# Kernel tuning notes

Measured on AMD Instinct MI355X. Metric: run time of the kernel, lower is better.

Reference implementation:

```python
import jax, jax.numpy as jnp
import numpy as np

NEG_INF = -1e30


def setup_inputs() -> dict:
    key = jax.random.key(0)
    ks = jax.random.split(key, 11)
    b, n, d = 4, 2048, 1024
    scale = 1.0 / np.sqrt(d)
    inp = {
        "q": jax.random.normal(ks[0], (b, n, d), jnp.float32),
        "k": jax.random.normal(ks[1], (b, n, d), jnp.float32),
        "v": jax.random.normal(ks[2], (b, n, d), jnp.float32),
        # nn.Linear params: weight [out, in], bias [out]
        "Wq": jax.random.normal(ks[3], (d, d), jnp.float32) * scale,
        "bq": jnp.zeros((d,), jnp.float32),
        "Wk": jax.random.normal(ks[4], (d, d), jnp.float32) * scale,
        "bk": jnp.zeros((d,), jnp.float32),
        "Wv": jax.random.normal(ks[5], (d, d), jnp.float32) * scale,
        "bv": jnp.zeros((d,), jnp.float32),
        "Wo": jax.random.normal(ks[6], (d, d), jnp.float32) * scale,
        "bo": jnp.zeros((d,), jnp.float32),
    }
    return inp


def reference(q, k, v, Wq, bq, Wk, bk, Wv, bv, Wo, bo):
    # Faithful to source: the multi-head reshape/transpose results are never
    # assigned, so attention runs single-headed over full n_embd vectors.
    b, n, d = q.shape
    qp = q @ Wq.T + bq  # [b, n, d]
    kp = k @ Wk.T + bk
    vp = v @ Wv.T + bv
    scale = jnp.asarray(1.0 / d, qp.dtype) ** 0.5  # sqrt(1/d)
    att = jnp.einsum('bnd,bmd->bnm', qp, kp) * scale  # [b, n, n]
    causal = jnp.tril(jnp.ones((n, n), bool))          # block_size tril sliced to n
    att = jnp.where(causal[None, :, :], att, NEG_INF)
    att = jax.nn.softmax(att, axis=-1)  # dropout p=0.0 -> identity
    y = att @ vp                        # [b, n, d]
    # source bug reproduced: transpose(1,2) then reshape(b, n, d)
    y = jnp.swapaxes(y, 1, 2).reshape(b, n, d)
    y = y @ Wo.T + bo
    return y
```

## Files before the change

kernel.cpp:

```cpp
#include <hip/hip_runtime.h>
#include <hip/hip_bf16.h>
#include <stdint.h>

typedef __bf16 bf16_t;
typedef __bf16 bf16x8 __attribute__((ext_vector_type(8)));
typedef __bf16 bf16x4 __attribute__((ext_vector_type(4)));
typedef float f32x4 __attribute__((ext_vector_type(4)));

#define GLD_LDS16(src, dst)                                                              \
  __builtin_amdgcn_global_load_lds((const __attribute__((address_space(1))) void*)(src), \
                                   (__attribute__((address_space(3))) void*)(dst), 16, 0, 0)

struct CvtArgs {
  const float* src[7];
  bf16_t* dst[7];
  long n4[7];
};

__global__ __launch_bounds__(256) void cvt_all(CvtArgs a) {
  const int seg = blockIdx.y;
  const float* __restrict__ in = a.src[seg];
  bf16_t* __restrict__ out = a.dst[seg];
  const long n4 = a.n4[seg];
  long i = (long)blockIdx.x * blockDim.x + threadIdx.x;
  const long stride = (long)gridDim.x * blockDim.x;
  for (; i < n4; i += stride) {
    float4 v = ((const float4*)in)[i];
    bf16x4 o;
    o[0] = (bf16_t)v.x; o[1] = (bf16_t)v.y; o[2] = (bf16_t)v.z; o[3] = (bf16_t)v.w;
    ((bf16x4*)out)[i] = o;
  }
}

__global__ __launch_bounds__(256) void transpose_bf16(const bf16_t* __restrict__ in,
                                                      bf16_t* __restrict__ out,
                                                      int rows, int cols, long sIn, long sOut) {
  __shared__ bf16_t tile[32][33];
  const int z = blockIdx.z;
  in  += (long)z * sIn;
  out += (long)z * sOut;
  const int c0 = blockIdx.x << 5, r0 = blockIdx.y << 5;
  const int tc = threadIdx.x & 31, tr = threadIdx.x >> 5;
#pragma unroll
  for (int it = 0; it < 4; ++it)
    tile[tr + it * 8][tc] = in[(long)(r0 + tr + it * 8) * cols + c0 + tc];
  __syncthreads();
#pragma unroll
  for (int it = 0; it < 4; ++it)
    out[(long)(c0 + tr + it * 8) * rows + r0 + tc] = tile[tc][tr + it * 8];
}

__global__ __launch_bounds__(256) void softmax_causal(bf16_t* __restrict__ S, int n, long sB) {
  const int i = blockIdx.x;
  const int z = blockIdx.y;
  bf16_t* row = S + (long)z * sB + (long)i * n;
  const int t = threadIdx.x;
  const int j0 = t << 3;

  bf16x8 vv = ((const bf16x8*)row)[t];
  float vals[8];
  float mx = -3.0e38f;
#pragma unroll
  for (int e = 0; e < 8; ++e) {
    float v = (j0 + e <= i) ? (float)vv[e] : -3.0e38f;
    vals[e] = v;
    mx = fmaxf(mx, v);
  }
#pragma unroll
  for (int off = 32; off; off >>= 1) mx = fmaxf(mx, __shfl_xor(mx, off));
  __shared__ float redm[4];
  if ((t & 63) == 0) redm[t >> 6] = mx;
  __syncthreads();
  mx = fmaxf(fmaxf(redm[0], redm[1]), fmaxf(redm[2], redm[3]));

  float sum = 0.f;
#pragma unroll
  for (int e = 0; e < 8; ++e) {
    float p = (j0 + e <= i) ? __expf(vals[e] - mx) : 0.f;
    vals[e] = p;
    sum += p;
  }
#pragma unroll
  for (int off = 32; off; off >>= 1) sum += __shfl_xor(sum, off);
  __shared__ float reds[4];
  if ((t & 63) == 0) reds[t >> 6] = sum;
  __syncthreads();
  sum = reds[0] + reds[1] + reds[2] + reds[3];
  const float inv = 1.0f / sum;

  bf16x8 o;
#pragma unroll
  for (int e = 0; e < 8; ++e) o[e] = (bf16_t)(vals[e] * inv);
  ((bf16x8*)row)[t] = o;
}

template <bool BF16_OUT, bool BIAS, bool KBOUND>
__device__ __forceinline__ void gemm_body(const bf16_t* __restrict__ A,
                                          const bf16_t* __restrict__ B,
                                          const float* __restrict__ bias,
                                          void* __restrict__ Cout,
                                          int N, int K, float alpha,
                                          int m0, int n0) {
  int KT = K >> 5;
  if (KBOUND) {
    int kb = (n0 + 128) >> 5;
    if (kb < KT) KT = kb;
  }

  __shared__ __align__(16) bf16_t As[128 * 32];
  __shared__ __align__(16) bf16_t Bs[128 * 32];

  const int t = threadIdx.x;
  const int l = t & 63;
  const int w = t >> 6;
  const int wr = w >> 1, wc = w & 1;

  const int c0 = t, c1 = t + 256;
  const bf16_t* a_src0 = A + (long)(m0 + (c0 >> 2)) * K + ((c0 & 3) << 3);
  const bf16_t* a_src1 = A + (long)(m0 + (c1 >> 2)) * K + ((c1 & 3) << 3);
  const bf16_t* b_src0 = B + (long)(n0 + (c0 >> 2)) * K + ((c0 & 3) << 3);
  const bf16_t* b_src1 = B + (long)(n0 + (c1 >> 2)) * K + ((c1 & 3) << 3);
  char* const asb = (char*)As;
  char* const bsb = (char*)Bs;
  char* const a_dst0 = asb + w * 1024;
  char* const a_dst1 = asb + 4096 + w * 1024;
  char* const b_dst0 = bsb + w * 1024;
  char* const b_dst1 = bsb + 4096 + w * 1024;

  const int r16 = l & 15, kg = l >> 4;
  int aoff[4], boff[4];
#pragma unroll
  for (int mi = 0; mi < 4; ++mi) aoff[mi] = (((wr * 64 + mi * 16 + r16) * 32) + kg * 8) * 2;
#pragma unroll
  for (int ni = 0; ni < 4; ++ni) boff[ni] = (((wc * 64 + ni * 16 + r16) * 32) + kg * 8) * 2;

  f32x4 acc[4][4] = {};

  for (int kt = 0; kt < KT; ++kt) {
    __syncthreads();
    GLD_LDS16(a_src0, a_dst0);
    GLD_LDS16(a_src1, a_dst1);
    GLD_LDS16(b_src0, b_dst0);
    GLD_LDS16(b_src1, b_dst1);
    a_src0 += 32; a_src1 += 32; b_src0 += 32; b_src1 += 32;
    __syncthreads();

    bf16x8 af[4], bfr[4];
#pragma unroll
    for (int mi = 0; mi < 4; ++mi) af[mi] = *(const bf16x8*)(asb + aoff[mi]);
#pragma unroll
    for (int ni = 0; ni < 4; ++ni) bfr[ni] = *(const bf16x8*)(bsb + boff[ni]);
#pragma unroll
    for (int mi = 0; mi < 4; ++mi)
#pragma unroll
      for (int ni = 0; ni < 4; ++ni)
        acc[mi][ni] = __builtin_amdgcn_mfma_f32_16x16x32_bf16(af[mi], bfr[ni], acc[mi][ni], 0, 0, 0);
  }

  const int rowbase = m0 + wr * 64 + ((l >> 4) << 2);
  const int colbase = n0 + wc * 64 + (l & 15);
  if constexpr (BF16_OUT) {
    bf16_t* C = (bf16_t*)Cout;
#pragma unroll
    for (int mi = 0; mi < 4; ++mi)
#pragma unroll
      for (int ni = 0; ni < 4; ++ni) {
        const int col = colbase + ni * 16;
        float badd = 0.f;
        if constexpr (BIAS) badd = bias[col];
#pragma unroll
        for (int j = 0; j < 4; ++j) {
          float v = acc[mi][ni][j] * alpha + badd;
          C[(long)(rowbase + mi * 16 + j) * N + col] = (bf16_t)v;
        }
      }
  } else {
    float* C = (float*)Cout;
#pragma unroll
    for (int mi = 0; mi < 4; ++mi)
#pragma unroll
      for (int ni = 0; ni < 4; ++ni) {
        const int col = colbase + ni * 16;
        float badd = 0.f;
        if constexpr (BIAS) badd = bias[col];
#pragma unroll
        for (int j = 0; j < 4; ++j) {
          float v = acc[mi][ni][j] * alpha + badd;
          C[(long)(rowbase + mi * 16 + j) * N + col] = v;
        }
      }
  }
}

__device__ __forceinline__ void xcd_remap(int& bx, int& by, int& bz) {
  const int gx = gridDim.x, gy = gridDim.y;
  int lin = (blockIdx.z * gy + blockIdx.y) * gx + blockIdx.x;
  const int nwg = gx * gy * (int)gridDim.z;
  lin = (lin & 7) * (nwg >> 3) + (lin >> 3);
  bx = lin % gx;
  const int rem = lin / gx;
  by = rem % gy;
  bz = rem / gy;
}

template <bool BF16_OUT, bool BIAS, bool CAUSAL_SKIP, bool KBOUND>
__global__ __launch_bounds__(256, 4) void gemm_bt(const bf16_t* __restrict__ A,
                                                  const bf16_t* __restrict__ B,
                                                  const float* __restrict__ bias,
                                                  void* __restrict__ Cout,
                                                  int N, int K, float alpha,
                                                  long sAb, long sBb, long sCb, int eltC) {
  int bx, by, bz;
  xcd_remap(bx, by, bz);
  const int m0 = by << 7, n0 = bx << 7;
  if (CAUSAL_SKIP && n0 > m0 + 127) return;
  gemm_body<BF16_OUT, BIAS, KBOUND>(A + (long)bz * sAb, B + (long)bz * sBb, bias,
                                    (char*)Cout + (long)bz * sCb * eltC, N, K, alpha, m0, n0);
}

struct QkvArgs {
  const bf16_t* A[3];
  const bf16_t* B[3];
  const float* bias[3];
  bf16_t* C[3];
};

__global__ __launch_bounds__(256, 4) void gemm_qkv(QkvArgs a, int N, int K) {
  int bx, by, bz;
  xcd_remap(bx, by, bz);
  gemm_body<true, true, false>(a.A[bz], a.B[bz], a.bias[bz], a.C[bz], N, K, 1.0f,
                               by << 7, bx << 7);
}

extern "C" void kernel_launch(void* const* d_in, const int* in_sizes, int n_in,
                              void* d_out, int out_size, void* d_ws, size_t ws_size,
                              hipStream_t stream) {
  const int b = 4, n = 2048, d = 1024;
  const long nd  = (long)n * d;
  const long bn  = (long)b * n;
  const long bnd = bn * d;
  const long ddl = (long)d * d;
  const long nn  = (long)n * n;

  const float* q  = (const float*)d_in[0];
  const float* k  = (const float*)d_in[1];
  const float* v  = (const float*)d_in[2];
  const float* Wq = (const float*)d_in[3];
  const float* bq = (const float*)d_in[4];
  const float* Wk = (const float*)d_in[5];
  const float* bk = (const float*)d_in[6];
  const float* Wv = (const float*)d_in[7];
  const float* bv = (const float*)d_in[8];
  const float* Wo = (const float*)d_in[9];
  const float* bo = (const float*)d_in[10];

  bf16_t* ws  = (bf16_t*)d_ws;
  bf16_t* qB  = ws;
  bf16_t* kB  = qB + bnd;
  bf16_t* vB  = kB + bnd;
  bf16_t* WqB = vB + bnd;
  bf16_t* WkB = WqB + ddl;
  bf16_t* WvB = WkB + ddl;
  bf16_t* WoB = WvB + ddl;
  bf16_t* qpB = WoB + ddl;
  bf16_t* kpB = qpB + bnd;
  bf16_t* vpB = kpB + bnd;
  bf16_t* vpT = vpB + bnd;
  bf16_t* S   = vpT + bnd;
  bf16_t* yT  = S + (long)b * nn;
  const size_t need = (size_t)(8 * bnd + 4 * ddl + (long)b * nn) * 2;
  if (ws_size < need) return;

  dim3 blk(256);

  CvtArgs ca;
  ca.src[0] = q;  ca.dst[0] = qB;  ca.n4[0] = bnd / 4;
  ca.src[1] = k;  ca.dst[1] = kB;  ca.n4[1] = bnd / 4;
  ca.src[2] = v;  ca.dst[2] = vB;  ca.n4[2] = bnd / 4;
  ca.src[3] = Wq; ca.dst[3] = WqB; ca.n4[3] = ddl / 4;
  ca.src[4] = Wk; ca.dst[4] = WkB; ca.n4[4] = ddl / 4;
  ca.src[5] = Wv; ca.dst[5] = WvB; ca.n4[5] = ddl / 4;
  ca.src[6] = Wo; ca.dst[6] = WoB; ca.n4[6] = ddl / 4;
  cvt_all<<<dim3(512, 7), blk, 0, stream>>>(ca);

  QkvArgs qa;
  qa.A[0] = qB; qa.B[0] = WqB; qa.bias[0] = bq; qa.C[0] = qpB;
  qa.A[1] = kB; qa.B[1] = WkB; qa.bias[1] = bk; qa.C[1] = kpB;
  qa.A[2] = vB; qa.B[2] = WvB; qa.bias[2] = bv; qa.C[2] = vpB;
  gemm_qkv<<<dim3(d / 128, bn / 128, 3), blk, 0, stream>>>(qa, d, d);

  transpose_bf16<<<dim3(d / 32, n / 32, b), blk, 0, stream>>>(vpB, vpT, n, d, nd, nd);

  gemm_bt<true, false, true, false><<<dim3(n / 128, n / 128, b), blk, 0, stream>>>(
      qpB, kpB, nullptr, S, n, d, 0.03125f, nd, nd, nn, 2);

  softmax_causal<<<dim3(n, b), blk, 0, stream>>>(S, n, nn);

  gemm_bt<true, false, false, true><<<dim3(n / 128, d / 128, b), blk, 0, stream>>>(
      vpT, S, nullptr, yT, n, n, 1.f, nd, nn, nd, 2);

  gemm_bt<false, true, false, false><<<dim3(d / 128, bn / 128, 1), blk, 0, stream>>>(
      yT, WoB, bo, (float*)d_out, d, d, 1.f, 0, 0, 0, 4);
}
```

Baseline: 221.9 us.

## Add 256x256 pipelined 8-wave GEMM for QKV and QK^T, fuse V transpose

Introduces a new 512-thread GEMM kernel using 256x256 output tiles, a 128KB double-buffered LDS staging scheme with swizzled offsets, explicit vmcnt waits and barriers, and setprio around MFMA bursts. It is used for the QKV projection and the causal QK^T scores. The V projection epilogue now writes the transposed layout directly, which removes the separate transpose kernel and its buffer. Larger tiles raise operand reuse and cut global traffic, but they lower occupancy and make causal skipping coarser.

```diff
diff --git a/kernel.cpp b/kernel.cpp
--- a/kernel.cpp
+++ b/kernel.cpp
@@ -10,6 +10,13 @@
 #define GLD_LDS16(src, dst)                                                              \
   __builtin_amdgcn_global_load_lds((const __attribute__((address_space(1))) void*)(src), \
                                    (__attribute__((address_space(3))) void*)(dst), 16, 0, 0)
+
+#define BAR() __builtin_amdgcn_s_barrier()
+#define LGKM0() asm volatile("s_waitcnt lgkmcnt(0)" ::: "memory")
+#define VMC6() asm volatile("s_waitcnt vmcnt(6)" ::: "memory")
+#define VMC0() asm volatile("s_waitcnt vmcnt(0)" ::: "memory")
+
+__device__ __forceinline__ int swz(int x) { return x ^ (((x >> 9) & 1) << 5); }
 
 struct CvtArgs {
   const float* src[7];
@@ -32,24 +39,6 @@
   }
 }
 
-__global__ __launch_bounds__(256) void transpose_bf16(const bf16_t* __restrict__ in,
-                                                      bf16_t* __restrict__ out,
-                                                      int rows, int cols, long sIn, long sOut) {
-  __shared__ bf16_t tile[32][33];
-  const int z = blockIdx.z;
-  in  += (long)z * sIn;
-  out += (long)z * sOut;
-  const int c0 = blockIdx.x << 5, r0 = blockIdx.y << 5;
-  const int tc = threadIdx.x & 31, tr = threadIdx.x >> 5;
-#pragma unroll
-  for (int it = 0; it < 4; ++it)
-    tile[tr + it * 8][tc] = in[(long)(r0 + tr + it * 8) * cols + c0 + tc];
-  __syncthreads();
-#pragma unroll
-  for (int it = 0; it < 4; ++it)
-    out[(long)(c0 + tr + it * 8) * rows + r0 + tc] = tile[tc][tr + it * 8];
-}
-
 __global__ __launch_bounds__(256) void softmax_causal(bf16_t* __restrict__ S, int n, long sB) {
   const int i = blockIdx.x;
   const int z = blockIdx.y;
@@ -92,6 +81,235 @@
 #pragma unroll
   for (int e = 0; e < 8; ++e) o[e] = (bf16_t)(vals[e] * inv);
   ((bf16x8*)row)[t] = o;
+}
+
+__device__ __forceinline__ void xcd_remap(int& bx, int& by, int& bz) {
+  const int gx = gridDim.x, gy = gridDim.y;
+  int lin = (blockIdx.z * gy + blockIdx.y) * gx + blockIdx.x;
+  const int nwg = gx * gy * (int)gridDim.z;
+  lin = (lin & 7) * (nwg >> 3) + (lin >> 3);
+  bx = lin % gx;
+  const int rem = lin / gx;
+  by = rem % gy;
+  bz = rem / gy;
+}
+
+struct G8Args {
+  const bf16_t* A[3];
+  const bf16_t* W[3];
+  const float* bias[3];
+  bf16_t* C[3];
+  long sA, sB, sC;
+};
+
+template <int HALF, int BUF>
+__device__ __forceinline__ void stage8(char* lds, const bf16_t* srcH, const int (&soff)[2],
+                                       int wid, int tile) {
+  const bf16_t* s = srcH + tile * 64;
+  char* d = lds + (HALF >= 2 ? 65536 : 0) + BUF * 32768 + (HALF & 1) * 16384 + wid * 2048;
+  GLD_LDS16(s + soff[0], d);
+  GLD_LDS16(s + soff[1], d + 1024);
+}
+
+template <int BUF, int QM>
+__device__ __forceinline__ void rdA(char* lds, const int (&aoffp)[4][2], bf16x8 (&af)[4][2]) {
+  char* b = lds + BUF * 32768 + QM * 16384;
+#pragma unroll
+  for (int mi = 0; mi < 4; ++mi)
+#pragma unroll
+    for (int kk = 0; kk < 2; ++kk) af[mi][kk] = *(const bf16x8*)(b + aoffp[mi][kk]);
+}
+
+template <int BUF, int QN>
+__device__ __forceinline__ void rdB(char* lds, const int (&boffp)[2][2], bf16x8 (&bf)[2][2]) {
+  char* b = lds + 65536 + BUF * 32768 + QN * 16384;
+#pragma unroll
+  for (int ni = 0; ni < 2; ++ni)
+#pragma unroll
+    for (int kk = 0; kk < 2; ++kk) bf[ni][kk] = *(const bf16x8*)(b + boffp[ni][kk]);
+}
+
+template <int QM, int QN>
+__device__ __forceinline__ void mm16(f32x4 (&acc)[2][2][4][2], const bf16x8 (&af)[4][2],
+                                     const bf16x8 (&bf)[2][2]) {
+  __builtin_amdgcn_s_setprio(1);
+#pragma unroll
+  for (int mi = 0; mi < 4; ++mi)
+#pragma unroll
+    for (int ni = 0; ni < 2; ++ni)
+#pragma unroll
+      for (int kk = 0; kk < 2; ++kk)
+        acc[QM][QN][mi][ni] = __builtin_amdgcn_mfma_f32_16x16x32_bf16(
+            af[mi][kk], bf[ni][kk], acc[QM][QN][mi][ni], 0, 0, 0);
+  __builtin_amdgcn_s_setprio(0);
+}
+
+template <int MODE>
+__global__ __launch_bounds__(512, 2) void gemm8(G8Args ga) {
+  int bx, by, bz;
+  xcd_remap(bx, by, bz);
+  const int m0 = by << 8, n0 = bx << 8;
+  if (MODE == 1 && n0 > m0 + 255) return;
+
+  const int K = 1024, NT = 16;
+  const bf16_t* A;
+  const bf16_t* B;
+  const float* bias = nullptr;
+  if (MODE == 0) {
+    A = ga.A[bz]; B = ga.W[bz]; bias = ga.bias[bz];
+  } else {
+    A = ga.A[0] + (long)bz * ga.sA;
+    B = ga.W[0] + (long)bz * ga.sB;
+  }
+
+  __shared__ __align__(16) char lds[131072];
+
+  const int t = threadIdx.x;
+  const int wid = t >> 6, l = t & 63;
+  const int wm = wid >> 2, wn = wid & 3;
+  const int ri16 = l & 15, kg = l >> 4;
+
+  int soff[2];
+#pragma unroll
+  for (int i = 0; i < 2; ++i) {
+    const int sub = wid * 2 + i;
+    const int ri = l >> 2;
+    const int cq = (l & 3) ^ ((ri & 8) >> 2);
+    const int r = (sub >> 1) * 16 + ri;
+    const int c = (sub & 1) * 32 + cq * 8;
+    soff[i] = r * K + c;
+  }
+  const bf16_t* srcA0 = A + (long)m0 * K;
+  const bf16_t* srcA1 = A + (long)(m0 + 128) * K;
+  const bf16_t* srcB0 = B + (long)n0 * K;
+  const bf16_t* srcB1 = B + (long)(n0 + 128) * K;
+
+  int aoffp[4][2], boffp[2][2];
+#pragma unroll
+  for (int mi = 0; mi < 4; ++mi)
+#pragma unroll
+    for (int kk = 0; kk < 2; ++kk)
+      aoffp[mi][kk] = swz((wm * 4 + mi) * 2048 + kk * 1024 + ri16 * 64 + kg * 16);
+#pragma unroll
+  for (int ni = 0; ni < 2; ++ni)
+#pragma unroll
+    for (int kk = 0; kk < 2; ++kk)
+      boffp[ni][kk] = swz((wn * 2 + ni) * 2048 + kk * 1024 + ri16 * 64 + kg * 16);
+
+  f32x4 acc[2][2][4][2] = {};
+  bf16x8 af[4][2], bf0[2][2], bf1[2][2];
+
+  stage8<0, 0>(lds, srcA0, soff, wid, 0);
+  stage8<2, 0>(lds, srcB0, soff, wid, 0);
+  stage8<3, 0>(lds, srcB1, soff, wid, 0);
+  stage8<1, 0>(lds, srcA1, soff, wid, 0);
+  stage8<0, 1>(lds, srcA0, soff, wid, 1);
+  stage8<2, 1>(lds, srcB0, soff, wid, 1);
+  stage8<3, 1>(lds, srcB1, soff, wid, 1);
+  VMC6();
+  BAR();
+
+  for (int tt = 0; tt < NT; tt += 2) {
+    const bool hasNext = (tt + 2) < NT;
+    rdA<0, 0>(lds, aoffp, af);
+    rdB<0, 0>(lds, boffp, bf0);
+    stage8<1, 1>(lds, srcA1, soff, wid, tt + 1);
+    BAR(); LGKM0();
+    mm16<0, 0>(acc, af, bf0);
+    BAR();
+    rdB<0, 1>(lds, boffp, bf1);
+    if (hasNext) stage8<0, 0>(lds, srcA0, soff, wid, tt + 2);
+    BAR(); LGKM0();
+    mm16<0, 1>(acc, af, bf1);
+    BAR();
+    rdA<0, 1>(lds, aoffp, af);
+    if (hasNext) stage8<2, 0>(lds, srcB0, soff, wid, tt + 2);
+    BAR(); LGKM0();
+    mm16<1, 0>(acc, af, bf0);
+    BAR();
+    if (hasNext) stage8<3, 0>(lds, srcB1, soff, wid, tt + 2);
+    BAR(); LGKM0();
+    mm16<1, 1>(acc, af, bf1);
+    if (hasNext) { VMC6(); } else { VMC0(); }
+    BAR();
+    rdA<1, 0>(lds, aoffp, af);
+    rdB<1, 0>(lds, boffp, bf0);
+    if (hasNext) stage8<1, 0>(lds, srcA1, soff, wid, tt + 2);
+    BAR(); LGKM0();
+    mm16<0, 0>(acc, af, bf0);
+    BAR();
+    rdB<1, 1>(lds, boffp, bf1);
+    if (hasNext) stage8<0, 1>(lds, srcA0, soff, wid, tt + 3);
+    BAR(); LGKM0();
+    mm16<0, 1>(acc, af, bf1);
+    BAR();
+    rdA<1, 1>(lds, aoffp, af);
+    if (hasNext) stage8<2, 1>(lds, srcB0, soff, wid, tt + 3);
+    BAR(); LGKM0();
+    mm16<1, 0>(acc, af, bf0);
+    BAR();
+    if (hasNext) stage8<3, 1>(lds, srcB1, soff, wid, tt + 3);
+    BAR(); LGKM0();
+    mm16<1, 1>(acc, af, bf1);
+    if (hasNext) { VMC6(); }
+    BAR();
+  }
+
+  if (MODE == 0) {
+    if (bz < 2) {
+      bf16_t* C = ga.C[bz];
+#pragma unroll
+      for (int qm = 0; qm < 2; ++qm)
+#pragma unroll
+        for (int qn = 0; qn < 2; ++qn)
+#pragma unroll
+          for (int mi = 0; mi < 4; ++mi)
+#pragma unroll
+            for (int ni = 0; ni < 2; ++ni) {
+              const int col = n0 + qn * 128 + wn * 32 + ni * 16 + ri16;
+              const int row0 = m0 + qm * 128 + wm * 64 + mi * 16 + kg * 4;
+              const float badd = bias[col];
+#pragma unroll
+              for (int j = 0; j < 4; ++j)
+                C[(long)(row0 + j) * 1024 + col] = (bf16_t)(acc[qm][qn][mi][ni][j] + badd);
+            }
+    } else {
+      bf16_t* C = ga.C[2];
+#pragma unroll
+      for (int qm = 0; qm < 2; ++qm)
+#pragma unroll
+        for (int qn = 0; qn < 2; ++qn)
+#pragma unroll
+          for (int mi = 0; mi < 4; ++mi)
+#pragma unroll
+            for (int ni = 0; ni < 2; ++ni) {
+              const int col = n0 + qn * 128 + wn * 32 + ni * 16 + ri16;
+              const int row0 = m0 + qm * 128 + wm * 64 + mi * 16 + kg * 4;
+              const float badd = bias[col];
+              const int batch = row0 >> 11, nr = row0 & 2047;
+              bf16x4 o;
+#pragma unroll
+              for (int j = 0; j < 4; ++j) o[j] = (bf16_t)(acc[qm][qn][mi][ni][j] + badd);
+              *(bf16x4*)(C + (long)batch * (2048 * 1024) + (long)col * 2048 + nr) = o;
+            }
+    }
+  } else {
+    bf16_t* C = ga.C[0] + (long)bz * ga.sC;
+#pragma unroll
+    for (int qm = 0; qm < 2; ++qm)
+#pragma unroll
+      for (int qn = 0; qn < 2; ++qn)
+#pragma unroll
+        for (int mi = 0; mi < 4; ++mi)
+#pragma unroll
+          for (int ni = 0; ni < 2; ++ni) {
+            const int col = n0 + qn * 128 + wn * 32 + ni * 16 + ri16;
+            const int row0 = m0 + qm * 128 + wm * 64 + mi * 16 + kg * 4;
+#pragma unroll
+            for (int j = 0; j < 4; ++j)
+              C[(long)(row0 + j) * 2048 + col] = (bf16_t)(acc[qm][qn][mi][ni][j] * 0.03125f);
+          }
+  }
 }
 
 template <bool BF16_OUT, bool BIAS, bool KBOUND>
@@ -192,18 +410,7 @@
   }
 }
 
-__device__ __forceinline__ void xcd_remap(int& bx, int& by, int& bz) {
-  const int gx = gridDim.x, gy = gridDim.y;
-  int lin = (blockIdx.z * gy + blockIdx.y) * gx + blockIdx.x;
-  const int nwg = gx * gy * (int)gridDim.z;
-  lin = (lin & 7) * (nwg >> 3) + (lin >> 3);
-  bx = lin % gx;
-  const int rem = lin / gx;
-  by = rem % gy;
-  bz = rem / gy;
-}
-
-template <bool BF16_OUT, bool BIAS, bool CAUSAL_SKIP, bool KBOUND>
+template <bool BF16_OUT, bool BIAS, bool KBOUND>
 __global__ __launch_bounds__(256, 4) void gemm_bt(const bf16_t* __restrict__ A,
                                                   const bf16_t* __restrict__ B,
                                                   const float* __restrict__ bias,
@@ -213,23 +420,8 @@
   int bx, by, bz;
   xcd_remap(bx, by, bz);
   const int m0 = by << 7, n0 = bx << 7;
-  if (CAUSAL_SKIP && n0 > m0 + 127) return;
   gemm_body<BF16_OUT, BIAS, KBOUND>(A + (long)bz * sAb, B + (long)bz * sBb, bias,
                                     (char*)Cout + (long)bz * sCb * eltC, N, K, alpha, m0, n0);
-}
-
-struct QkvArgs {
-  const bf16_t* A[3];
-  const bf16_t* B[3];
-  const float* bias[3];
-  bf16_t* C[3];
-};
-
-__global__ __launch_bounds__(256, 4) void gemm_qkv(QkvArgs a, int N, int K) {
-  int bx, by, bz;
-  xcd_remap(bx, by, bz);
-  gemm_body<true, true, false>(a.A[bz], a.B[bz], a.bias[bz], a.C[bz], N, K, 1.0f,
-                               by << 7, bx << 7);
 }
 
 extern "C" void kernel_launch(void* const* d_in, const int* in_sizes, int n_in,
@@ -264,11 +456,10 @@
   bf16_t* WoB = WvB + ddl;
   bf16_t* qpB = WoB + ddl;
   bf16_t* kpB = qpB + bnd;
-  bf16_t* vpB = kpB + bnd;
-  bf16_t* vpT = vpB + bnd;
+  bf16_t* vpT = kpB + bnd;
   bf16_t* S   = vpT + bnd;
   bf16_t* yT  = S + (long)b * nn;
-  const size_t need = (size_t)(8 * bnd + 4 * ddl + (long)b * nn) * 2;
+  const size_t need = (size_t)(7 * bnd + 4 * ddl + (long)b * nn) * 2;
   if (ws_size < need) return;
 
   dim3 blk(256);
@@ -283,22 +474,22 @@
   ca.src[6] = Wo; ca.dst[6] = WoB; ca.n4[6] = ddl / 4;
   cvt_all<<<dim3(512, 7), blk, 0, stream>>>(ca);
 
-  QkvArgs qa;
-  qa.A[0] = qB; qa.B[0] = WqB; qa.bias[0] = bq; qa.C[0] = qpB;
-  qa.A[1] = kB; qa.B[1] = WkB; qa.bias[1] = bk; qa.C[1] = kpB;
-  qa.A[2] = vB; qa.B[2] = WvB; qa.bias[2] = bv; qa.C[2] = vpB;
-  gemm_qkv<<<dim3(d / 128, bn / 128, 3), blk, 0, stream>>>(qa, d, d);
-
-  transpose_bf16<<<dim3(d / 32, n / 32, b), blk, 0, stream>>>(vpB, vpT, n, d, nd, nd);
-
-  gemm_bt<true, false, true, false><<<dim3(n / 128, n / 128, b), blk, 0, stream>>>(
-      qpB, kpB, nullptr, S, n, d, 0.03125f, nd, nd, nn, 2);
+  G8Args qa = {};
+  qa.A[0] = qB; qa.W[0] = WqB; qa.bias[0] = bq; qa.C[0] = qpB;
+  qa.A[1] = kB; qa.W[1] = WkB; qa.bias[1] = bk; qa.C[1] = kpB;
+  qa.A[2] = vB; qa.W[2] = WvB; qa.bias[2] = bv; qa.C[2] = vpT;
+  gemm8<0><<<dim3(d / 256, bn / 256, 3), dim3(512), 0, stream>>>(qa);
+
+  G8Args sa = {};
+  sa.A[0] = qpB; sa.W[0] = kpB; sa.C[0] = S;
+  sa.sA = nd; sa.sB = nd; sa.sC = nn;
+  gemm8<1><<<dim3(n / 256, n / 256, b), dim3(512), 0, stream>>>(sa);
 
   softmax_causal<<<dim3(n, b), blk, 0, stream>>>(S, n, nn);
 
-  gemm_bt<true, false, false, true><<<dim3(n / 128, d / 128, b), blk, 0, stream>>>(
+  gemm_bt<true, false, true><<<dim3(n / 128, d / 128, b), blk, 0, stream>>>(
       vpT, S, nullptr, yT, n, n, 1.f, nd, nn, nd, 2);
 
-  gemm_bt<false, true, false, false><<<dim3(d / 128, bn / 128, 1), blk, 0, stream>>>(
+  gemm_bt<false, true, false><<<dim3(d / 128, bn / 128, 1), blk, 0, stream>>>(
       yT, WoB, bo, (float*)d_out, d, d, 1.f, 0, 0, 0, 4);
 }
```

Measured after the change: 220.9 us. About the same (-0.4%).

## Fuse fp32-to-bf16 activation conversion and V transpose into QKV GEMM

Applied to the files above, without the earlier changes.

The QKV projection GEMM now loads fp32 activations straight into LDS with direct global-to-LDS loads and converts them to bf16 on the fly. This removes the separate conversion pass over q, k and v and its intermediate bf16 buffers. The V projection writes its output already transposed, so the standalone transpose kernel is dropped. Softmax also skips loading and storing columns beyond the causal 128-block boundary. In exchange, the GEMM moves twice the A-operand bytes through LDS and does extra conversion work inside the inner loop.

```diff
diff --git a/kernel.cpp b/kernel.cpp
--- a/kernel.cpp
+++ b/kernel.cpp
@@ -12,9 +12,9 @@
                                    (__attribute__((address_space(3))) void*)(dst), 16, 0, 0)
 
 struct CvtArgs {
-  const float* src[7];
-  bf16_t* dst[7];
-  long n4[7];
+  const float* src[4];
+  bf16_t* dst[4];
+  long n4[4];
 };
 
 __global__ __launch_bounds__(256) void cvt_all(CvtArgs a) {
@@ -32,39 +32,25 @@
   }
 }
 
-__global__ __launch_bounds__(256) void transpose_bf16(const bf16_t* __restrict__ in,
-                                                      bf16_t* __restrict__ out,
-                                                      int rows, int cols, long sIn, long sOut) {
-  __shared__ bf16_t tile[32][33];
-  const int z = blockIdx.z;
-  in  += (long)z * sIn;
-  out += (long)z * sOut;
-  const int c0 = blockIdx.x << 5, r0 = blockIdx.y << 5;
-  const int tc = threadIdx.x & 31, tr = threadIdx.x >> 5;
-#pragma unroll
-  for (int it = 0; it < 4; ++it)
-    tile[tr + it * 8][tc] = in[(long)(r0 + tr + it * 8) * cols + c0 + tc];
-  __syncthreads();
-#pragma unroll
-  for (int it = 0; it < 4; ++it)
-    out[(long)(c0 + tr + it * 8) * rows + r0 + tc] = tile[tc][tr + it * 8];
-}
-
 __global__ __launch_bounds__(256) void softmax_causal(bf16_t* __restrict__ S, int n, long sB) {
   const int i = blockIdx.x;
   const int z = blockIdx.y;
   bf16_t* row = S + (long)z * sB + (long)i * n;
   const int t = threadIdx.x;
   const int j0 = t << 3;
-
-  bf16x8 vv = ((const bf16x8*)row)[t];
+  const int jmax = ((i >> 7) + 1) << 7;
+  const bool active = j0 < jmax;
+
   float vals[8];
   float mx = -3.0e38f;
-#pragma unroll
-  for (int e = 0; e < 8; ++e) {
-    float v = (j0 + e <= i) ? (float)vv[e] : -3.0e38f;
-    vals[e] = v;
-    mx = fmaxf(mx, v);
+  if (active) {
+    bf16x8 vv = ((const bf16x8*)row)[t];
+#pragma unroll
+    for (int e = 0; e < 8; ++e) {
+      float v = (j0 + e <= i) ? (float)vv[e] : -3.0e38f;
+      vals[e] = v;
+      mx = fmaxf(mx, v);
+    }
   }
 #pragma unroll
   for (int off = 32; off; off >>= 1) mx = fmaxf(mx, __shfl_xor(mx, off));
@@ -74,11 +60,13 @@
   mx = fmaxf(fmaxf(redm[0], redm[1]), fmaxf(redm[2], redm[3]));
 
   float sum = 0.f;
-#pragma unroll
-  for (int e = 0; e < 8; ++e) {
-    float p = (j0 + e <= i) ? __expf(vals[e] - mx) : 0.f;
-    vals[e] = p;
-    sum += p;
+  if (active) {
+#pragma unroll
+    for (int e = 0; e < 8; ++e) {
+      float p = (j0 + e <= i) ? __expf(vals[e] - mx) : 0.f;
+      vals[e] = p;
+      sum += p;
+    }
   }
 #pragma unroll
   for (int off = 32; off; off >>= 1) sum += __shfl_xor(sum, off);
@@ -88,19 +76,41 @@
   sum = reds[0] + reds[1] + reds[2] + reds[3];
   const float inv = 1.0f / sum;
 
-  bf16x8 o;
-#pragma unroll
-  for (int e = 0; e < 8; ++e) o[e] = (bf16_t)(vals[e] * inv);
-  ((bf16x8*)row)[t] = o;
-}
-
-template <bool BF16_OUT, bool BIAS, bool KBOUND>
-__device__ __forceinline__ void gemm_body(const bf16_t* __restrict__ A,
-                                          const bf16_t* __restrict__ B,
-                                          const float* __restrict__ bias,
-                                          void* __restrict__ Cout,
-                                          int N, int K, float alpha,
-                                          int m0, int n0) {
+  if (active) {
+    bf16x8 o;
+#pragma unroll
+    for (int e = 0; e < 8; ++e) o[e] = (bf16_t)(vals[e] * inv);
+    ((bf16x8*)row)[t] = o;
+  }
+}
+
+__device__ __forceinline__ void xcd_remap(int& bx, int& by, int& bz) {
+  const int gx = gridDim.x, gy = gridDim.y;
+  int lin = (blockIdx.z * gy + blockIdx.y) * gx + blockIdx.x;
+  const int nwg = gx * gy * (int)gridDim.z;
+  lin = (lin & 7) * (nwg >> 3) + (lin >> 3);
+  bx = lin % gx;
+  const int rem = lin / gx;
+  by = rem % gy;
+  bz = rem / gy;
+}
+
+template <bool BF16_OUT, bool BIAS, bool CAUSAL_SKIP, bool KBOUND>
+__global__ __launch_bounds__(256, 4) void gemm_bt(const bf16_t* __restrict__ Ag,
+                                                  const bf16_t* __restrict__ Bg,
+                                                  const float* __restrict__ bias,
+                                                  void* __restrict__ Cout,
+                                                  int N, int K, float alpha,
+                                                  long sAb, long sBb, long sCb, int eltC) {
+  int bx, by, bz;
+  xcd_remap(bx, by, bz);
+  const int m0 = by << 7, n0 = bx << 7;
+  if (CAUSAL_SKIP && n0 > m0 + 127) return;
+
+  const bf16_t* A = Ag + (long)bz * sAb;
+  const bf16_t* B = Bg + (long)bz * sBb;
+  void* Cv = (char*)Cout + (long)bz * sCb * eltC;
+
   int KT = K >> 5;
   if (KBOUND) {
     int kb = (n0 + 128) >> 5;
@@ -160,7 +170,7 @@
   const int rowbase = m0 + wr * 64 + ((l >> 4) << 2);
   const int colbase = n0 + wc * 64 + (l & 15);
   if constexpr (BF16_OUT) {
-    bf16_t* C = (bf16_t*)Cout;
+    bf16_t* C = (bf16_t*)Cv;
 #pragma unroll
     for (int mi = 0; mi < 4; ++mi)
 #pragma unroll
@@ -175,7 +185,7 @@
         }
       }
   } else {
-    float* C = (float*)Cout;
+    float* C = (float*)Cv;
 #pragma unroll
     for (int mi = 0; mi < 4; ++mi)
 #pragma unroll
@@ -192,44 +202,119 @@
   }
 }
 
-__device__ __forceinline__ void xcd_remap(int& bx, int& by, int& bz) {
-  const int gx = gridDim.x, gy = gridDim.y;
-  int lin = (blockIdx.z * gy + blockIdx.y) * gx + blockIdx.x;
-  const int nwg = gx * gy * (int)gridDim.z;
-  lin = (lin & 7) * (nwg >> 3) + (lin >> 3);
-  bx = lin % gx;
-  const int rem = lin / gx;
-  by = rem % gy;
-  bz = rem / gy;
-}
-
-template <bool BF16_OUT, bool BIAS, bool CAUSAL_SKIP, bool KBOUND>
-__global__ __launch_bounds__(256, 4) void gemm_bt(const bf16_t* __restrict__ A,
-                                                  const bf16_t* __restrict__ B,
-                                                  const float* __restrict__ bias,
-                                                  void* __restrict__ Cout,
-                                                  int N, int K, float alpha,
-                                                  long sAb, long sBb, long sCb, int eltC) {
+struct QkvArgsF {
+  const float* A[3];
+  const bf16_t* W[3];
+  const float* bias[3];
+  bf16_t* C[3];
+};
+
+__global__ __launch_bounds__(256, 4) void gemm_qkv_f32dma(QkvArgsF ga, int N, int K) {
   int bx, by, bz;
   xcd_remap(bx, by, bz);
   const int m0 = by << 7, n0 = bx << 7;
-  if (CAUSAL_SKIP && n0 > m0 + 127) return;
-  gemm_body<BF16_OUT, BIAS, KBOUND>(A + (long)bz * sAb, B + (long)bz * sBb, bias,
-                                    (char*)Cout + (long)bz * sCb * eltC, N, K, alpha, m0, n0);
-}
-
-struct QkvArgs {
-  const bf16_t* A[3];
-  const bf16_t* B[3];
-  const float* bias[3];
-  bf16_t* C[3];
-};
-
-__global__ __launch_bounds__(256, 4) void gemm_qkv(QkvArgs a, int N, int K) {
-  int bx, by, bz;
-  xcd_remap(bx, by, bz);
-  gemm_body<true, true, false>(a.A[bz], a.B[bz], a.bias[bz], a.C[bz], N, K, 1.0f,
-                               by << 7, bx << 7);
+
+  const float* __restrict__ A = ga.A[bz];
+  const bf16_t* __restrict__ B = ga.W[bz];
+  const float* __restrict__ bias = ga.bias[bz];
+  const int KT = K >> 5;
+
+  __shared__ __align__(16) char lds[24576];
+  char* const asb = lds;
+  char* const bsb = lds + 16384;
+
+  const int t = threadIdx.x;
+  const int l = t & 63;
+  const int w = t >> 6;
+  const int wr = w >> 1, wc = w & 1;
+
+  const float* a_src[4];
+#pragma unroll
+  for (int i = 0; i < 4; ++i) {
+    const int c = i * 256 + t;
+    const int row = c >> 3;
+    const int lo16 = (c & 7) ^ (row & 7);
+    a_src[i] = A + (long)(m0 + row) * K + lo16 * 4;
+  }
+  const int c0 = t, c1 = t + 256;
+  const bf16_t* b_src0 = B + (long)(n0 + (c0 >> 2)) * K + ((c0 & 3) << 3);
+  const bf16_t* b_src1 = B + (long)(n0 + (c1 >> 2)) * K + ((c1 & 3) << 3);
+  char* const b_dst0 = bsb + w * 1024;
+  char* const b_dst1 = bsb + 4096 + w * 1024;
+
+  const int r16 = l & 15, kg = l >> 4;
+  int aoff[4], boff[4];
+#pragma unroll
+  for (int mi = 0; mi < 4; ++mi) {
+    const int row = wr * 64 + mi * 16 + r16;
+    aoff[mi] = (row * 128 + kg * 32) ^ ((row & 7) << 4);
+  }
+#pragma unroll
+  for (int ni = 0; ni < 4; ++ni) boff[ni] = (((wc * 64 + ni * 16 + r16) * 32) + kg * 8) * 2;
+
+  f32x4 acc[4][4] = {};
+
+  for (int kt = 0; kt < KT; ++kt) {
+    __syncthreads();
+#pragma unroll
+    for (int i = 0; i < 4; ++i) {
+      GLD_LDS16(a_src[i], asb + i * 4096 + w * 1024);
+      a_src[i] += 32;
+    }
+    GLD_LDS16(b_src0, b_dst0);
+    GLD_LDS16(b_src1, b_dst1);
+    b_src0 += 32; b_src1 += 32;
+    __syncthreads();
+
+    bf16x8 af[4], bfr[4];
+#pragma unroll
+    for (int mi = 0; mi < 4; ++mi) {
+      f32x4 lo4 = *(const f32x4*)(asb + aoff[mi]);
+      f32x4 hi4 = *(const f32x4*)(asb + (aoff[mi] ^ 16));
+      af[mi][0] = (bf16_t)lo4[0]; af[mi][1] = (bf16_t)lo4[1];
+      af[mi][2] = (bf16_t)lo4[2]; af[mi][3] = (bf16_t)lo4[3];
+      af[mi][4] = (bf16_t)hi4[0]; af[mi][5] = (bf16_t)hi4[1];
+      af[mi][6] = (bf16_t)hi4[2]; af[mi][7] = (bf16_t)hi4[3];
+    }
+#pragma unroll
+    for (int ni = 0; ni < 4; ++ni) bfr[ni] = *(const bf16x8*)(bsb + boff[ni]);
+#pragma unroll
+    for (int mi = 0; mi < 4; ++mi)
+#pragma unroll
+      for (int ni = 0; ni < 4; ++ni)
+        acc[mi][ni] = __builtin_amdgcn_mfma_f32_16x16x32_bf16(af[mi], bfr[ni], acc[mi][ni], 0, 0, 0);
+  }
+
+  const int rowbase = m0 + wr * 64 + ((l >> 4) << 2);
+  const int colbase = n0 + wc * 64 + (l & 15);
+  if (bz < 2) {
+    bf16_t* C = ga.C[bz];
+#pragma unroll
+    for (int mi = 0; mi < 4; ++mi)
+#pragma unroll
+      for (int ni = 0; ni < 4; ++ni) {
+        const int col = colbase + ni * 16;
+        const float badd = bias[col];
+#pragma unroll
+        for (int j = 0; j < 4; ++j)
+          C[(long)(rowbase + mi * 16 + j) * N + col] = (bf16_t)(acc[mi][ni][j] + badd);
+      }
+  } else {
+    bf16_t* C = ga.C[2];
+#pragma unroll
+    for (int mi = 0; mi < 4; ++mi)
+#pragma unroll
+      for (int ni = 0; ni < 4; ++ni) {
+        const int col = colbase + ni * 16;
+        const float badd = bias[col];
+        const int row0 = rowbase + mi * 16;
+        const int batch = row0 >> 11, nr = row0 & 2047;
+        bf16x4 o;
+#pragma unroll
+        for (int j = 0; j < 4; ++j) o[j] = (bf16_t)(acc[mi][ni][j] + badd);
+        *(bf16x4*)(C + (long)batch * (2048 * 1024) + (long)col * 2048 + nr) = o;
+      }
+  }
 }
 
 extern "C" void kernel_launch(void* const* d_in, const int* in_sizes, int n_in,
@@ -255,41 +340,32 @@
   const float* bo = (const float*)d_in[10];
 
   bf16_t* ws  = (bf16_t*)d_ws;
-  bf16_t* qB  = ws;
-  bf16_t* kB  = qB + bnd;
-  bf16_t* vB  = kB + bnd;
-  bf16_t* WqB = vB + bnd;
+  bf16_t* WqB = ws;
   bf16_t* WkB = WqB + ddl;
   bf16_t* WvB = WkB + ddl;
   bf16_t* WoB = WvB + ddl;
   bf16_t* qpB = WoB + ddl;
   bf16_t* kpB = qpB + bnd;
-  bf16_t* vpB = kpB + bnd;
-  bf16_t* vpT = vpB + bnd;
+  bf16_t* vpT = kpB + bnd;
   bf16_t* S   = vpT + bnd;
   bf16_t* yT  = S + (long)b * nn;
-  const size_t need = (size_t)(8 * bnd + 4 * ddl + (long)b * nn) * 2;
+  const size_t need = (size_t)(4 * ddl + 4 * bnd + (long)b * nn) * 2;
   if (ws_size < need) return;
 
   dim3 blk(256);
 
   CvtArgs ca;
-  ca.src[0] = q;  ca.dst[0] = qB;  ca.n4[0] = bnd / 4;
-  ca.src[1] = k;  ca.dst[1] = kB;  ca.n4[1] = bnd / 4;
-  ca.src[2] = v;  ca.dst[2] = vB;  ca.n4[2] = bnd / 4;
-  ca.src[3] = Wq; ca.dst[3] = WqB; ca.n4[3] = ddl / 4;
-  ca.src[4] = Wk; ca.dst[4] = WkB; ca.n4[4] = ddl / 4;
-  ca.src[5] = Wv; ca.dst[5] = WvB; ca.n4[5] = ddl / 4;
-  ca.src[6] = Wo; ca.dst[6] = WoB; ca.n4[6] = ddl / 4;
-  cvt_all<<<dim3(512, 7), blk, 0, stream>>>(ca);
-
-  QkvArgs qa;
-  qa.A[0] = qB; qa.B[0] = WqB; qa.bias[0] = bq; qa.C[0] = qpB;
-  qa.A[1] = kB; qa.B[1] = WkB; qa.bias[1] = bk; qa.C[1] = kpB;
-  qa.A[2] = vB; qa.B[2] = WvB; qa.bias[2] = bv; qa.C[2] = vpB;
-  gemm_qkv<<<dim3(d / 128, bn / 128, 3), blk, 0, stream>>>(qa, d, d);
-
-  transpose_bf16<<<dim3(d / 32, n / 32, b), blk, 0, stream>>>(vpB, vpT, n, d, nd, nd);
+  ca.src[0] = Wq; ca.dst[0] = WqB; ca.n4[0] = ddl / 4;
+  ca.src[1] = Wk; ca.dst[1] = WkB; ca.n4[1] = ddl / 4;
+  ca.src[2] = Wv; ca.dst[2] = WvB; ca.n4[2] = ddl / 4;
+  ca.src[3] = Wo; ca.dst[3] = WoB; ca.n4[3] = ddl / 4;
+  cvt_all<<<dim3(256, 4), blk, 0, stream>>>(ca);
+
+  QkvArgsF qa;
+  qa.A[0] = q; qa.W[0] = WqB; qa.bias[0] = bq; qa.C[0] = qpB;
+  qa.A[1] = k; qa.W[1] = WkB; qa.bias[1] = bk; qa.C[1] = kpB;
+  qa.A[2] = v; qa.W[2] = WvB; qa.bias[2] = bv; qa.C[2] = vpT;
+  gemm_qkv_f32dma<<<dim3(d / 128, bn / 128, 3), blk, 0, stream>>>(qa, d, d);
 
   gemm_bt<true, false, true, false><<<dim3(n / 128, n / 128, b), blk, 0, stream>>>(
       qpB, kpB, nullptr, S, n, d, 0.03125f, nd, nd, nn, 2);
```

Measured after the change: 211.5 us. -4.7%, faster.

## Fuse V projection with transposed store into QK^T launch, drop transpose kernel

Applied to the files above, without the earlier changes.

The V projection now runs inside the same launch as the causal QK^T score GEMM, using extra z-slices of the grid, and writes its result directly in transposed layout through a new epilogue. This removes the separate transpose kernel and the intermediate vp buffer. Softmax now skips loading and storing columns beyond the causal 128-block boundary. The transposed epilogue writes 4-element strided chunks, which may coalesce less well than row-major stores.

```diff
diff --git a/kernel.cpp b/kernel.cpp
--- a/kernel.cpp
+++ b/kernel.cpp
@@ -32,39 +32,25 @@
   }
 }
 
-__global__ __launch_bounds__(256) void transpose_bf16(const bf16_t* __restrict__ in,
-                                                      bf16_t* __restrict__ out,
-                                                      int rows, int cols, long sIn, long sOut) {
-  __shared__ bf16_t tile[32][33];
-  const int z = blockIdx.z;
-  in  += (long)z * sIn;
-  out += (long)z * sOut;
-  const int c0 = blockIdx.x << 5, r0 = blockIdx.y << 5;
-  const int tc = threadIdx.x & 31, tr = threadIdx.x >> 5;
-#pragma unroll
-  for (int it = 0; it < 4; ++it)
-    tile[tr + it * 8][tc] = in[(long)(r0 + tr + it * 8) * cols + c0 + tc];
-  __syncthreads();
-#pragma unroll
-  for (int it = 0; it < 4; ++it)
-    out[(long)(c0 + tr + it * 8) * rows + r0 + tc] = tile[tc][tr + it * 8];
-}
-
 __global__ __launch_bounds__(256) void softmax_causal(bf16_t* __restrict__ S, int n, long sB) {
   const int i = blockIdx.x;
   const int z = blockIdx.y;
   bf16_t* row = S + (long)z * sB + (long)i * n;
   const int t = threadIdx.x;
   const int j0 = t << 3;
-
-  bf16x8 vv = ((const bf16x8*)row)[t];
+  const int jmax = ((i >> 7) + 1) << 7;
+  const bool active = j0 < jmax;
+
   float vals[8];
   float mx = -3.0e38f;
-#pragma unroll
-  for (int e = 0; e < 8; ++e) {
-    float v = (j0 + e <= i) ? (float)vv[e] : -3.0e38f;
-    vals[e] = v;
-    mx = fmaxf(mx, v);
+  if (active) {
+    bf16x8 vv = ((const bf16x8*)row)[t];
+#pragma unroll
+    for (int e = 0; e < 8; ++e) {
+      float v = (j0 + e <= i) ? (float)vv[e] : -3.0e38f;
+      vals[e] = v;
+      mx = fmaxf(mx, v);
+    }
   }
 #pragma unroll
   for (int off = 32; off; off >>= 1) mx = fmaxf(mx, __shfl_xor(mx, off));
@@ -74,11 +60,13 @@
   mx = fmaxf(fmaxf(redm[0], redm[1]), fmaxf(redm[2], redm[3]));
 
   float sum = 0.f;
-#pragma unroll
-  for (int e = 0; e < 8; ++e) {
-    float p = (j0 + e <= i) ? __expf(vals[e] - mx) : 0.f;
-    vals[e] = p;
-    sum += p;
+  if (active) {
+#pragma unroll
+    for (int e = 0; e < 8; ++e) {
+      float p = (j0 + e <= i) ? __expf(vals[e] - mx) : 0.f;
+      vals[e] = p;
+      sum += p;
+    }
   }
 #pragma unroll
   for (int off = 32; off; off >>= 1) sum += __shfl_xor(sum, off);
@@ -88,13 +76,26 @@
   sum = reds[0] + reds[1] + reds[2] + reds[3];
   const float inv = 1.0f / sum;
 
-  bf16x8 o;
-#pragma unroll
-  for (int e = 0; e < 8; ++e) o[e] = (bf16_t)(vals[e] * inv);
-  ((bf16x8*)row)[t] = o;
-}
-
-template <bool BF16_OUT, bool BIAS, bool KBOUND>
+  if (active) {
+    bf16x8 o;
+#pragma unroll
+    for (int e = 0; e < 8; ++e) o[e] = (bf16_t)(vals[e] * inv);
+    ((bf16x8*)row)[t] = o;
+  }
+}
+
+__device__ __forceinline__ void xcd_remap(int& bx, int& by, int& bz) {
+  const int gx = gridDim.x, gy = gridDim.y;
+  int lin = (blockIdx.z * gy + blockIdx.y) * gx + blockIdx.x;
+  const int nwg = gx * gy * (int)gridDim.z;
+  lin = (lin & 7) * (nwg >> 3) + (lin >> 3);
+  bx = lin % gx;
+  const int rem = lin / gx;
+  by = rem % gy;
+  bz = rem / gy;
+}
+
+template <int EPI, bool BIAS, bool KBOUND>
 __device__ __forceinline__ void gemm_body(const bf16_t* __restrict__ A,
                                           const bf16_t* __restrict__ B,
                                           const float* __restrict__ bias,
@@ -159,8 +160,8 @@
 
   const int rowbase = m0 + wr * 64 + ((l >> 4) << 2);
   const int colbase = n0 + wc * 64 + (l & 15);
-  if constexpr (BF16_OUT) {
-    bf16_t* C = (bf16_t*)Cout;
+  if constexpr (EPI == 0) {
+    float* C = (float*)Cout;
 #pragma unroll
     for (int mi = 0; mi < 4; ++mi)
 #pragma unroll
@@ -169,13 +170,11 @@
         float badd = 0.f;
         if constexpr (BIAS) badd = bias[col];
 #pragma unroll
-        for (int j = 0; j < 4; ++j) {
-          float v = acc[mi][ni][j] * alpha + badd;
-          C[(long)(rowbase + mi * 16 + j) * N + col] = (bf16_t)v;
-        }
+        for (int j = 0; j < 4; ++j)
+          C[(long)(rowbase + mi * 16 + j) * N + col] = acc[mi][ni][j] * alpha + badd;
       }
-  } else {
-    float* C = (float*)Cout;
+  } else if constexpr (EPI == 1) {
+    bf16_t* C = (bf16_t*)Cout;
 #pragma unroll
     for (int mi = 0; mi < 4; ++mi)
 #pragma unroll
@@ -184,28 +183,31 @@
         float badd = 0.f;
         if constexpr (BIAS) badd = bias[col];
 #pragma unroll
-        for (int j = 0; j < 4; ++j) {
-          float v = acc[mi][ni][j] * alpha + badd;
-          C[(long)(rowbase + mi * 16 + j) * N + col] = v;
-        }
+        for (int j = 0; j < 4; ++j)
+          C[(long)(rowbase + mi * 16 + j) * N + col] = (bf16_t)(acc[mi][ni][j] * alpha + badd);
       }
-  }
-}
-
-__device__ __forceinline__ void xcd_remap(int& bx, int& by, int& bz) {
-  const int gx = gridDim.x, gy = gridDim.y;
-  int lin = (blockIdx.z * gy + blockIdx.y) * gx + blockIdx.x;
-  const int nwg = gx * gy * (int)gridDim.z;
-  lin = (lin & 7) * (nwg >> 3) + (lin >> 3);
-  bx = lin % gx;
-  const int rem = lin / gx;
-  by = rem % gy;
-  bz = rem / gy;
-}
-
-template <bool BF16_OUT, bool BIAS, bool CAUSAL_SKIP, bool KBOUND>
-__global__ __launch_bounds__(256, 4) void gemm_bt(const bf16_t* __restrict__ A,
-                                                  const bf16_t* __restrict__ B,
+  } else {
+    bf16_t* C = (bf16_t*)Cout;
+#pragma unroll
+    for (int mi = 0; mi < 4; ++mi)
+#pragma unroll
+      for (int ni = 0; ni < 4; ++ni) {
+        const int col = colbase + ni * 16;
+        float badd = 0.f;
+        if constexpr (BIAS) badd = bias[col];
+        const int row0 = rowbase + mi * 16;
+        const int batch = row0 >> 11, nr = row0 & 2047;
+        bf16x4 o;
+#pragma unroll
+        for (int j = 0; j < 4; ++j) o[j] = (bf16_t)(acc[mi][ni][j] + badd);
+        *(bf16x4*)(C + (long)batch * (2048 * 1024) + (long)col * 2048 + nr) = o;
+      }
+  }
+}
+
+template <int EPI, bool BIAS, bool KBOUND>
+__global__ __launch_bounds__(256, 4) void gemm_bt(const bf16_t* __restrict__ Ag,
+                                                  const bf16_t* __restrict__ Bg,
                                                   const float* __restrict__ bias,
                                                   void* __restrict__ Cout,
                                                   int N, int K, float alpha,
@@ -213,23 +215,48 @@
   int bx, by, bz;
   xcd_remap(bx, by, bz);
   const int m0 = by << 7, n0 = bx << 7;
-  if (CAUSAL_SKIP && n0 > m0 + 127) return;
-  gemm_body<BF16_OUT, BIAS, KBOUND>(A + (long)bz * sAb, B + (long)bz * sBb, bias,
-                                    (char*)Cout + (long)bz * sCb * eltC, N, K, alpha, m0, n0);
-}
-
-struct QkvArgs {
-  const bf16_t* A[3];
-  const bf16_t* B[3];
-  const float* bias[3];
-  bf16_t* C[3];
+  gemm_body<EPI, BIAS, KBOUND>(Ag + (long)bz * sAb, Bg + (long)bz * sBb, bias,
+                               (char*)Cout + (long)bz * sCb * eltC, N, K, alpha, m0, n0);
+}
+
+struct QkArgs {
+  const bf16_t* A[2];
+  const bf16_t* W[2];
+  const float* bias[2];
+  bf16_t* C[2];
 };
 
-__global__ __launch_bounds__(256, 4) void gemm_qkv(QkvArgs a, int N, int K) {
+__global__ __launch_bounds__(256, 4) void gemm_qk(QkArgs a, int N, int K) {
   int bx, by, bz;
   xcd_remap(bx, by, bz);
-  gemm_body<true, true, false>(a.A[bz], a.B[bz], a.bias[bz], a.C[bz], N, K, 1.0f,
-                               by << 7, bx << 7);
+  gemm_body<1, true, false>(a.A[bz], a.W[bz], a.bias[bz], a.C[bz], N, K, 1.0f,
+                            by << 7, bx << 7);
+}
+
+struct FsvArgs {
+  const bf16_t* qp;
+  const bf16_t* kp;
+  bf16_t* S;
+  const bf16_t* vB;
+  const bf16_t* Wv;
+  const float* bv;
+  bf16_t* vpT;
+  long nd, nn;
+};
+
+__global__ __launch_bounds__(256, 4) void fused_sv(FsvArgs a) {
+  int bx, by, bz;
+  xcd_remap(bx, by, bz);
+  if (bz < 4) {
+    const int m0 = by << 7, n0 = bx << 7;
+    if (n0 > m0 + 127) return;
+    gemm_body<1, false, false>(a.qp + (long)bz * a.nd, a.kp + (long)bz * a.nd, nullptr,
+                               a.S + (long)bz * a.nn, 2048, 1024, 0.03125f, m0, n0);
+  } else {
+    const int lin = (bz - 4) * 256 + by * 16 + bx;
+    const int m0 = (lin >> 3) << 7, n0 = (lin & 7) << 7;
+    gemm_body<2, true, false>(a.vB, a.Wv, a.bv, a.vpT, 1024, 1024, 1.0f, m0, n0);
+  }
 }
 
 extern "C" void kernel_launch(void* const* d_in, const int* in_sizes, int n_in,
@@ -264,11 +291,10 @@
   bf16_t* WoB = WvB + ddl;
   bf16_t* qpB = WoB + ddl;
   bf16_t* kpB = qpB + bnd;
-  bf16_t* vpB = kpB + bnd;
-  bf16_t* vpT = vpB + bnd;
+  bf16_t* vpT = kpB + bnd;
   bf16_t* S   = vpT + bnd;
   bf16_t* yT  = S + (long)b * nn;
-  const size_t need = (size_t)(8 * bnd + 4 * ddl + (long)b * nn) * 2;
+  const size_t need = (size_t)(7 * bnd + 4 * ddl + (long)b * nn) * 2;
   if (ws_size < need) return;
 
   dim3 blk(256);
@@ -283,22 +309,22 @@
   ca.src[6] = Wo; ca.dst[6] = WoB; ca.n4[6] = ddl / 4;
   cvt_all<<<dim3(512, 7), blk, 0, stream>>>(ca);
 
-  QkvArgs qa;
-  qa.A[0] = qB; qa.B[0] = WqB; qa.bias[0] = bq; qa.C[0] = qpB;
-  qa.A[1] = kB; qa.B[1] = WkB; qa.bias[1] = bk; qa.C[1] = kpB;
-  qa.A[2] = vB; qa.B[2] = WvB; qa.bias[2] = bv; qa.C[2] = vpB;
-  gemm_qkv<<<dim3(d / 128, bn / 128, 3), blk, 0, stream>>>(qa, d, d);
-
-  transpose_bf16<<<dim3(d / 32, n / 32, b), blk, 0, stream>>>(vpB, vpT, n, d, nd, nd);
-
-  gemm_bt<true, false, true, false><<<dim3(n / 128, n / 128, b), blk, 0, stream>>>(
-      qpB, kpB, nullptr, S, n, d, 0.03125f, nd, nd, nn, 2);
+  QkArgs qa;
+  qa.A[0] = qB; qa.W[0] = WqB; qa.bias[0] = bq; qa.C[0] = qpB;
+  qa.A[1] = kB; qa.W[1] = WkB; qa.bias[1] = bk; qa.C[1] = kpB;
+  gemm_qk<<<dim3(d / 128, bn / 128, 2), blk, 0, stream>>>(qa, d, d);
+
+  FsvArgs fa;
+  fa.qp = qpB; fa.kp = kpB; fa.S = S;
+  fa.vB = vB; fa.Wv = WvB; fa.bv = bv; fa.vpT = vpT;
+  fa.nd = nd; fa.nn = nn;
+  fused_sv<<<dim3(16, 16, 6), blk, 0, stream>>>(fa);
 
   softmax_causal<<<dim3(n, b), blk, 0, stream>>>(S, n, nn);
 
-  gemm_bt<true, false, false, true><<<dim3(n / 128, d / 128, b), blk, 0, stream>>>(
+  gemm_bt<1, false, true><<<dim3(n / 128, d / 128, b), blk, 0, stream>>>(
       vpT, S, nullptr, yT, n, n, 1.f, nd, nn, nd, 2);
 
-  gemm_bt<false, true, false, false><<<dim3(d / 128, bn / 128, 1), blk, 0, stream>>>(
+  gemm_bt<0, true, false><<<dim3(d / 128, bn / 128, 1), blk, 0, stream>>>(
       yT, WoB, bo, (float*)d_out, d, d, 1.f, 0, 0, 0, 4);
 }
```

After: 218.5 us. No clear change (-1.5%).
